# Optimization experiments

Measured on AMD Instinct MI355X. Metric: run time of the kernel, lower is better.

Reference implementation:

```python
import jax, jax.numpy as jnp
import numpy as np

DIM = 512
HEADS = 8
DK = DIM // HEADS
MAX_LEN = 22118
EPS = 1e-5


def _layernorm(h, g, b):
    m = jnp.mean(h, axis=-1, keepdims=True)
    v = jnp.mean((h - m) ** 2, axis=-1, keepdims=True)
    return (h - m) / jnp.sqrt(v + EPS) * g + b


def setup_inputs() -> dict:
    key = jax.random.key(0)
    ks = jax.random.split(key, 16)
    B, S = 4, 2048
    xavier = lambda k, shp: jax.random.normal(k, shp, jnp.float32) * np.sqrt(2.0 / (shp[0] + shp[1]))
    return {
        "x": jax.random.normal(ks[0], (B, S, DIM), jnp.float32),
        "vis_data": jax.random.normal(ks[1], (B, S, DIM), jnp.float32),
        "coord1": jax.random.randint(ks[2], (B, S), 0, MAX_LEN, jnp.int32),
        "coord2": jax.random.randint(ks[3], (B, S), 0, MAX_LEN, jnp.int32),
        "emb1": jax.random.normal(ks[4], (MAX_LEN, DIM // 2), jnp.float32) * 0.02,
        "emb2": jax.random.normal(ks[5], (MAX_LEN, DIM // 2), jnp.float32) * 0.02,
        "wq": xavier(ks[6], (DIM, DIM)), "bq": jnp.zeros((DIM,), jnp.float32),
        "wk": xavier(ks[7], (DIM, DIM)), "bk": jnp.zeros((DIM,), jnp.float32),
        "wv": xavier(ks[8], (DIM, DIM)), "bv": jnp.zeros((DIM,), jnp.float32),
        "w1": xavier(ks[9], (DIM, DIM)), "b1": jnp.zeros((DIM,), jnp.float32),
        "g1": jnp.ones((DIM,), jnp.float32), "beta1": jnp.zeros((DIM,), jnp.float32),
        "w2": xavier(ks[10], (DIM, DIM)), "b2": jnp.zeros((DIM,), jnp.float32),
        "g2": jnp.ones((DIM,), jnp.float32), "beta2": jnp.zeros((DIM,), jnp.float32),
    }


def reference(x, vis_data, coord1, coord2, emb1, emb2, wq, bq, wk, bk, wv, bv,
              w1, b1, g1, beta1, w2, b2, g2, beta2):
    B, S, _ = x.shape
    # learned positional encoding: concat of two coordinate embeddings
    pos = jnp.concatenate([emb1[coord1], emb2[coord2]], axis=-1)  # [B,S,DIM]
    xp = x + pos
    # Q/K from vis_data, V from position-encoded x
    q = (vis_data @ wq + bq).reshape(B, S, HEADS, DK)
    k = (vis_data @ wk + bk).reshape(B, S, HEADS, DK)
    v = (xp @ wv + bv).reshape(B, S, HEADS, DK)
    scores = jnp.einsum("bqhd,bkhd->bhqk", q, k) / np.sqrt(DK).astype(np.float32)
    attn = jax.nn.softmax(scores, axis=-1)  # dropout is identity in eval
    out = jnp.einsum("bhqk,bkhd->bqhd", attn, v).reshape(B, S, DIM)
    # post-attention MLP stack (self.layer)
    h = jax.nn.leaky_relu(out @ w1 + b1, negative_slope=0.2)
    h = _layernorm(h, g1, beta1)
    h = jax.nn.leaky_relu(h @ w2 + b2, negative_slope=0.2)
    h = _layernorm(h, g2, beta2)
    return h
```

## Files before the change

kernel.cpp:

```cpp
#include <hip/hip_runtime.h>

#define DIM 512
#define SEQ 2048
#define MROWS 8192

typedef short short8 __attribute__((ext_vector_type(8)));
typedef float floatx4 __attribute__((ext_vector_type(4)));

__device__ __forceinline__ ushort f2bf(float f) {
  union { float f; unsigned u; } v; v.f = f;
  unsigned r = v.u + 0x7fff + ((v.u >> 16) & 1);
  return (ushort)(r >> 16);
}
__device__ __forceinline__ float bf2f(ushort u) {
  union { unsigned u; float f; } v; v.u = ((unsigned)u) << 16;
  return v.f;
}

__global__ __launch_bounds__(256) void prep_kernel(
    const float* __restrict__ x, const float* __restrict__ vis,
    const int* __restrict__ c1, const int* __restrict__ c2,
    const float* __restrict__ e1, const float* __restrict__ e2,
    ushort* __restrict__ xp_bf, ushort* __restrict__ vis_bf) {
  int gid = blockIdx.x * 256 + threadIdx.x;
  int row = gid >> 7;
  int col = (gid & 127) * 4;
  float4 vv = *(const float4*)(vis + (size_t)row * 512 + col);
  ushort4 vb; vb.x = f2bf(vv.x); vb.y = f2bf(vv.y); vb.z = f2bf(vv.z); vb.w = f2bf(vv.w);
  *(ushort4*)(vis_bf + (size_t)row * 512 + col) = vb;
  float4 p;
  if (col < 256) p = *(const float4*)(e1 + (size_t)c1[row] * 256 + col);
  else           p = *(const float4*)(e2 + (size_t)c2[row] * 256 + col - 256);
  float4 xv = *(const float4*)(x + (size_t)row * 512 + col);
  ushort4 xb; xb.x = f2bf(xv.x + p.x); xb.y = f2bf(xv.y + p.y);
  xb.z = f2bf(xv.z + p.z); xb.w = f2bf(xv.w + p.w);
  *(ushort4*)(xp_bf + (size_t)row * 512 + col) = xb;
}

__global__ __launch_bounds__(256) void wtrans_kernel(
    const float* __restrict__ wq, const float* __restrict__ wk,
    const float* __restrict__ wv, const float* __restrict__ w1,
    const float* __restrict__ w2,
    ushort* __restrict__ wt_qkv, ushort* __restrict__ wt1,
    ushort* __restrict__ wt2) {
  __shared__ float Ls[64 * 65];
  int mid = blockIdx.x >> 6;
  int tile = blockIdx.x & 63;
  int k0 = (tile >> 3) * 64, n0 = (tile & 7) * 64;
  const float* W = mid == 0 ? wq : mid == 1 ? wk : mid == 2 ? wv : mid == 3 ? w1 : w2;
  ushort* outp = mid < 3 ? (wt_qkv + (size_t)mid * 512 * 512) : (mid == 3 ? wt1 : wt2);
  float scale = (mid == 0) ? 0.125f : 1.0f;
  int r = threadIdx.x >> 4, c4 = (threadIdx.x & 15) * 4;
#pragma unroll
  for (int i = 0; i < 4; i++) {
    int row = i * 16 + r;
    float4 wv4 = *(const float4*)(W + (size_t)(k0 + row) * 512 + n0 + c4);
    Ls[row * 65 + c4 + 0] = wv4.x * scale;
    Ls[row * 65 + c4 + 1] = wv4.y * scale;
    Ls[row * 65 + c4 + 2] = wv4.z * scale;
    Ls[row * 65 + c4 + 3] = wv4.w * scale;
  }
  __syncthreads();
  int n = threadIdx.x >> 2, kc = (threadIdx.x & 3) * 16;
  ushort pk[16];
#pragma unroll
  for (int i = 0; i < 16; i++) pk[i] = f2bf(Ls[(kc + i) * 65 + n]);
  ushort* op = outp + (size_t)(n0 + n) * 512 + k0 + kc;
  *(uint4*)op = *(uint4*)pk;
  *(uint4*)(op + 8) = *(uint4*)(pk + 8);
}

template <bool LEAKY>
__global__ __launch_bounds__(256, 3) void gemm_mfma(
    const ushort* __restrict__ A01, const ushort* __restrict__ A2,
    const ushort* __restrict__ Wt,
    const float* __restrict__ bias0, const float* __restrict__ bias1,
    const float* __restrict__ bias2,
    ushort* __restrict__ out0, ushort* __restrict__ out1,
    ushort* __restrict__ out2, float s0scale) {
  __shared__ __align__(16) ushort As[128 * 64];
  __shared__ __align__(16) ushort Bs[128 * 64];
  int t = threadIdx.x;
  int seg = blockIdx.x >> 2;
  int nloc0 = (blockIdx.x & 3) * 128;
  int n0w = blockIdx.x * 128;
  int m0 = blockIdx.y * 128;
  const ushort* A = (seg < 2) ? A01 : A2;
  const float* bias = seg == 0 ? bias0 : seg == 1 ? bias1 : bias2;
  ushort* out = seg == 0 ? out0 : seg == 1 ? out1 : out2;
  float bscale = seg == 0 ? s0scale : 1.0f;

  int w = t >> 6, lane = t & 63;
  int wm = (w & 1) * 64, wn = (w >> 1) * 64;
  int quad = lane >> 4, lcol = lane & 15;
  int srow = t >> 3, sch = t & 7;

  floatx4 acc[4][4] = {};

  for (int k0 = 0; k0 < 512; k0 += 64) {
    __syncthreads();
#pragma unroll
    for (int i = 0; i < 4; i++) {
      int row = i * 32 + srow;
      int pofs = row * 64 + (sch ^ (row & 7)) * 8;
      *(uint4*)(&As[pofs]) =
          *(const uint4*)(A + (size_t)(m0 + row) * 512 + k0 + sch * 8);
      *(uint4*)(&Bs[pofs]) =
          *(const uint4*)(Wt + (size_t)(n0w + row) * 512 + k0 + sch * 8);
    }
    __syncthreads();
#pragma unroll
    for (int kc = 0; kc < 2; kc++) {
      int pch = ((kc * 4 + quad) ^ (lcol & 7)) * 8;
      short8 af[4], bfr[4];
#pragma unroll
      for (int i = 0; i < 4; i++) {
        af[i]  = *(const short8*)(&As[(wm + i * 16 + lcol) * 64 + pch]);
        bfr[i] = *(const short8*)(&Bs[(wn + i * 16 + lcol) * 64 + pch]);
      }
#pragma unroll
      for (int mt = 0; mt < 4; mt++)
#pragma unroll
        for (int nt = 0; nt < 4; nt++)
          acc[mt][nt] = __builtin_amdgcn_mfma_f32_16x16x32_bf16(
              af[mt], bfr[nt], acc[mt][nt], 0, 0, 0);
    }
  }

  __syncthreads();
  float* Ls = ((w & 2) ? (float*)Bs : (float*)As) + (w & 1) * 1104;
  int rr = lane >> 2, cc = (lane & 3) * 16;
#pragma unroll
  for (int mt = 0; mt < 4; mt++) {
#pragma unroll
    for (int nt = 0; nt < 4; nt++) {
      float bv = bias[nloc0 + wn + nt * 16 + lcol] * bscale;
#pragma unroll
      for (int r = 0; r < 4; r++) {
        float vv = acc[mt][nt][r] + bv;
        if (LEAKY) vv = vv >= 0.f ? vv : 0.2f * vv;
        Ls[(quad * 4 + r) * 68 + nt * 16 + lcol] = vv;
      }
    }
    asm volatile("s_waitcnt lgkmcnt(0)" ::: "memory");
    ushort pk[16];
#pragma unroll
    for (int i = 0; i < 16; i += 4) {
      float4 fv = *(const float4*)(&Ls[rr * 68 + cc + i]);
      pk[i] = f2bf(fv.x); pk[i + 1] = f2bf(fv.y);
      pk[i + 2] = f2bf(fv.z); pk[i + 3] = f2bf(fv.w);
    }
    ushort* op = out + (size_t)(m0 + wm + mt * 16 + rr) * 512 + nloc0 + wn + cc;
    *(uint4*)op = *(uint4*)pk;
    *(uint4*)(op + 8) = *(uint4*)(pk + 8);
    asm volatile("s_waitcnt lgkmcnt(0)" ::: "memory");
  }
}

__global__ __launch_bounds__(256, 4) void attn_mfma_kernel(
    const ushort* __restrict__ q, const ushort* __restrict__ k,
    const ushort* __restrict__ v, ushort* __restrict__ out) {
  __shared__ __align__(16) ushort Ks[128 * 64];
  __shared__ __align__(16) ushort Vt[64 * 128];
  __shared__ __align__(16) ushort Ps[4 * 16 * 64];
  int t = threadIdx.x;
  int blk = blockIdx.x;
  int qt = blk & 31, h = (blk >> 5) & 7, b = blk >> 8;
  int wave = t >> 6, lane = t & 63, quad = lane >> 4, lcol = lane & 15;
  int q0 = qt * 64 + wave * 16;
  const size_t base = (size_t)b * SEQ * 512 + h * 64;

  short8 qf[2];
#pragma unroll
  for (int kc = 0; kc < 2; kc++)
    qf[kc] = *(const short8*)(q + base + (size_t)(q0 + lcol) * 512 + kc * 32 + quad * 8);

  floatx4 O[4] = {};
  float lsum[4] = {0.f, 0.f, 0.f, 0.f};

  ushort* Pw = Ps + wave * (16 * 64);
  int krow = t >> 1, khalf = t & 1;
  int pl = t & 63, dg = t >> 6;

  for (int kt = 0; kt < SEQ; kt += 128) {
    __syncthreads();
#pragma unroll
    for (int j = 0; j < 4; j++) {
      int ch = khalf * 4 + j;
      *(uint4*)(&Ks[krow * 64 + (ch ^ (krow & 7)) * 8]) =
          *(const uint4*)(k + base + (size_t)(kt + krow) * 512 + ch * 8);
    }
    {
      uint4 va[2], vb[2];
      const ushort* vr0 = v + base + (size_t)(kt + 2 * pl) * 512 + dg * 16;
      const ushort* vr1 = vr0 + 512;
      va[0] = *(const uint4*)(vr0); va[1] = *(const uint4*)(vr0 + 8);
      vb[0] = *(const uint4*)(vr1); vb[1] = *(const uint4*)(vr1 + 8);
      const ushort* a0 = (const ushort*)va;
      const ushort* a1 = (const ushort*)vb;
#pragma unroll
      for (int i = 0; i < 16; i++) {
        int dim = dg * 16 + i;
        unsigned pack = (unsigned)a0[i] | ((unsigned)a1[i] << 16);
        int pch = (pl >> 2) ^ (dim & 7);
        *(unsigned*)(&Vt[dim * 128 + pch * 8 + (pl & 3) * 2]) = pack;
      }
    }
    __syncthreads();

    floatx4 S[8] = {};
#pragma unroll
    for (int kc = 0; kc < 2; kc++) {
      int pch = ((kc * 4 + quad) ^ (lcol & 7)) * 8;
#pragma unroll
      for (int jt = 0; jt < 8; jt++) {
        short8 kf = *(const short8*)(&Ks[(jt * 16 + lcol) * 64 + pch]);
        S[jt] = __builtin_amdgcn_mfma_f32_16x16x32_bf16(qf[kc], kf, S[jt], 0, 0, 0);
      }
    }

#pragma unroll
    for (int half = 0; half < 2; half++) {
#pragma unroll
      for (int jt4 = 0; jt4 < 4; jt4++) {
        int jt = half * 4 + jt4;
#pragma unroll
        for (int r = 0; r < 4; r++) {
          float p = __expf(S[jt][r]);
          lsum[r] += p;
          int prow = quad * 4 + r;
          int pcol = jt4 * 16 + lcol;
          int pch = (pcol >> 3) ^ (prow & 7);
          Pw[prow * 64 + pch * 8 + (pcol & 7)] =
              (ushort)(__float_as_uint(p) >> 16);
        }
      }
      asm volatile("s_waitcnt lgkmcnt(0)" ::: "memory");
#pragma unroll
      for (int kc = 0; kc < 2; kc++) {
        short8 pf = *(const short8*)(
            &Pw[lcol * 64 + ((kc * 4 + quad) ^ (lcol & 7)) * 8]);
#pragma unroll
        for (int nt = 0; nt < 4; nt++) {
          int dim = nt * 16 + lcol;
          int ch = half * 8 + kc * 4 + quad;
          short8 vf = *(const short8*)(&Vt[dim * 128 + (ch ^ (lcol & 7)) * 8]);
          O[nt] = __builtin_amdgcn_mfma_f32_16x16x32_bf16(pf, vf, O[nt], 0, 0, 0);
        }
      }
    }
  }

#pragma unroll
  for (int r = 0; r < 4; r++) {
#pragma unroll
    for (int m = 1; m <= 8; m <<= 1) lsum[r] += __shfl_xor(lsum[r], m, 64);
    lsum[r] = 1.f / lsum[r];
  }
#pragma unroll
  for (int nt = 0; nt < 4; nt++)
#pragma unroll
    for (int r = 0; r < 4; r++)
      out[base + (size_t)(q0 + quad * 4 + r) * 512 + nt * 16 + lcol] =
          f2bf(O[nt][r] * lsum[r]);
}

template <bool OUTF32>
__global__ __launch_bounds__(256) void ln_kernel(
    const ushort* __restrict__ h, const float* __restrict__ g,
    const float* __restrict__ beta, void* __restrict__ outv) {
  int wave = threadIdx.x >> 6, lane = threadIdx.x & 63;
  int row = blockIdx.x * 4 + wave;
  uint4 raw = *(const uint4*)(h + (size_t)row * 512 + lane * 8);
  const ushort* hu = (const ushort*)&raw;
  float vals[8];
#pragma unroll
  for (int i = 0; i < 8; i++) vals[i] = bf2f(hu[i]);
  float sum = 0.f;
#pragma unroll
  for (int i = 0; i < 8; i++) sum += vals[i];
#pragma unroll
  for (int off = 32; off >= 1; off >>= 1) sum += __shfl_xor(sum, off, 64);
  float mean = sum * (1.f / 512.f);
  float vs = 0.f;
#pragma unroll
  for (int i = 0; i < 8; i++) { float d = vals[i] - mean; vs += d * d; }
#pragma unroll
  for (int off = 32; off >= 1; off >>= 1) vs += __shfl_xor(vs, off, 64);
  float rstd = rsqrtf(vs * (1.f / 512.f) + 1e-5f);
  float4 gv0 = *(const float4*)(g + lane * 8);
  float4 gv1 = *(const float4*)(g + lane * 8 + 4);
  float4 bv0 = *(const float4*)(beta + lane * 8);
  float4 bv1 = *(const float4*)(beta + lane * 8 + 4);
  float gr[8] = {gv0.x, gv0.y, gv0.z, gv0.w, gv1.x, gv1.y, gv1.z, gv1.w};
  float br[8] = {bv0.x, bv0.y, bv0.z, bv0.w, bv1.x, bv1.y, bv1.z, bv1.w};
  float res[8];
#pragma unroll
  for (int i = 0; i < 8; i++) res[i] = (vals[i] - mean) * rstd * gr[i] + br[i];
  if (OUTF32) {
    float* op = (float*)outv + (size_t)row * 512 + lane * 8;
    float4 o0, o1;
    o0.x = res[0]; o0.y = res[1]; o0.z = res[2]; o0.w = res[3];
    o1.x = res[4]; o1.y = res[5]; o1.z = res[6]; o1.w = res[7];
    *(float4*)op = o0; *(float4*)(op + 4) = o1;
  } else {
    ushort* op = (ushort*)outv + (size_t)row * 512 + lane * 8;
    ushort4 o0, o1;
    o0.x = f2bf(res[0]); o0.y = f2bf(res[1]); o0.z = f2bf(res[2]); o0.w = f2bf(res[3]);
    o1.x = f2bf(res[4]); o1.y = f2bf(res[5]); o1.z = f2bf(res[6]); o1.w = f2bf(res[7]);
    *(ushort4*)op = o0; *(ushort4*)(op + 4) = o1;
  }
}

extern "C" void kernel_launch(void* const* d_in, const int* in_sizes, int n_in,
                              void* d_out, int out_size, void* d_ws,
                              size_t ws_size, hipStream_t stream) {
  (void)in_sizes; (void)n_in; (void)out_size; (void)ws_size;
  const float* x     = (const float*)d_in[0];
  const float* vis   = (const float*)d_in[1];
  const int*   c1    = (const int*)d_in[2];
  const int*   c2    = (const int*)d_in[3];
  const float* e1    = (const float*)d_in[4];
  const float* e2    = (const float*)d_in[5];
  const float* wq    = (const float*)d_in[6];
  const float* bq    = (const float*)d_in[7];
  const float* wk    = (const float*)d_in[8];
  const float* bk    = (const float*)d_in[9];
  const float* wv    = (const float*)d_in[10];
  const float* bv    = (const float*)d_in[11];
  const float* w1    = (const float*)d_in[12];
  const float* b1    = (const float*)d_in[13];
  const float* g1    = (const float*)d_in[14];
  const float* beta1 = (const float*)d_in[15];
  const float* w2    = (const float*)d_in[16];
  const float* b2    = (const float*)d_in[17];
  const float* g2    = (const float*)d_in[18];
  const float* beta2 = (const float*)d_in[19];
  float* out = (float*)d_out;
  ushort* ws = (ushort*)d_ws;

  const size_t BUF = (size_t)MROWS * 512;
  ushort* xp_bf  = ws;
  ushort* vis_bf = ws + BUF;
  ushort* q_bf   = ws + 2 * BUF;
  ushort* k_bf   = ws + 3 * BUF;
  ushort* v_bf   = ws + 4 * BUF;
  ushort* wt_qkv = ws + 5 * BUF;
  ushort* wt1    = wt_qkv + 1536 * 512;
  ushort* wt2    = wt1 + 512 * 512;
  ushort* attn_bf = vis_bf;
  ushort* h1_bf   = xp_bf;
  ushort* ln1_bf  = q_bf;
  ushort* h2_bf   = k_bf;

  prep_kernel<<<4096, 256, 0, stream>>>(x, vis, c1, c2, e1, e2, xp_bf, vis_bf);
  wtrans_kernel<<<320, 256, 0, stream>>>(wq, wk, wv, w1, w2, wt_qkv, wt1, wt2);
  gemm_mfma<false><<<dim3(12, 64), 256, 0, stream>>>(
      vis_bf, xp_bf, wt_qkv, bq, bk, bv, q_bf, k_bf, v_bf, 0.125f);
  attn_mfma_kernel<<<1024, 256, 0, stream>>>(q_bf, k_bf, v_bf, attn_bf);
  gemm_mfma<true><<<dim3(4, 64), 256, 0, stream>>>(
      attn_bf, attn_bf, wt1, b1, b1, b1, h1_bf, h1_bf, h1_bf, 1.0f);
  ln_kernel<false><<<2048, 256, 0, stream>>>(h1_bf, g1, beta1, ln1_bf);
  gemm_mfma<true><<<dim3(4, 64), 256, 0, stream>>>(
      ln1_bf, ln1_bf, wt2, b2, b2, b2, h2_bf, h2_bf, h2_bf, 1.0f);
  ln_kernel<true><<<2048, 256, 0, stream>>>(h2_bf, g2, beta2, out);
}
```

Before: 308.1 us.

## Double attention query tile per block, shrink GEMM M-tile, merge prep kernels

The attention kernel now processes 32 query rows per wave (128 per block), so each loaded K/V tile is reused across twice as many queries and the grid is halved. In exchange it uses more registers and LDS, and its launch bound drops to 2 blocks per SM. The GEMM M-tile shrinks from 128 to 64 rows, doubling the grid, cutting LDS use and raising occupancy to 4 blocks. The prep and weight-transpose kernels are merged into one launch to remove a kernel launch.

```diff
diff --git a/kernel.cpp b/kernel.cpp
--- a/kernel.cpp
+++ b/kernel.cpp
@@ -17,109 +17,116 @@
   return v.f;
 }
 
-__global__ __launch_bounds__(256) void prep_kernel(
+__global__ __launch_bounds__(256) void prep_wtrans_kernel(
     const float* __restrict__ x, const float* __restrict__ vis,
     const int* __restrict__ c1, const int* __restrict__ c2,
     const float* __restrict__ e1, const float* __restrict__ e2,
-    ushort* __restrict__ xp_bf, ushort* __restrict__ vis_bf) {
-  int gid = blockIdx.x * 256 + threadIdx.x;
-  int row = gid >> 7;
-  int col = (gid & 127) * 4;
-  float4 vv = *(const float4*)(vis + (size_t)row * 512 + col);
-  ushort4 vb; vb.x = f2bf(vv.x); vb.y = f2bf(vv.y); vb.z = f2bf(vv.z); vb.w = f2bf(vv.w);
-  *(ushort4*)(vis_bf + (size_t)row * 512 + col) = vb;
-  float4 p;
-  if (col < 256) p = *(const float4*)(e1 + (size_t)c1[row] * 256 + col);
-  else           p = *(const float4*)(e2 + (size_t)c2[row] * 256 + col - 256);
-  float4 xv = *(const float4*)(x + (size_t)row * 512 + col);
-  ushort4 xb; xb.x = f2bf(xv.x + p.x); xb.y = f2bf(xv.y + p.y);
-  xb.z = f2bf(xv.z + p.z); xb.w = f2bf(xv.w + p.w);
-  *(ushort4*)(xp_bf + (size_t)row * 512 + col) = xb;
-}
-
-__global__ __launch_bounds__(256) void wtrans_kernel(
     const float* __restrict__ wq, const float* __restrict__ wk,
     const float* __restrict__ wv, const float* __restrict__ w1,
     const float* __restrict__ w2,
+    ushort* __restrict__ xp_bf, ushort* __restrict__ vis_bf,
     ushort* __restrict__ wt_qkv, ushort* __restrict__ wt1,
     ushort* __restrict__ wt2) {
   __shared__ float Ls[64 * 65];
-  int mid = blockIdx.x >> 6;
-  int tile = blockIdx.x & 63;
-  int k0 = (tile >> 3) * 64, n0 = (tile & 7) * 64;
-  const float* W = mid == 0 ? wq : mid == 1 ? wk : mid == 2 ? wv : mid == 3 ? w1 : w2;
-  ushort* outp = mid < 3 ? (wt_qkv + (size_t)mid * 512 * 512) : (mid == 3 ? wt1 : wt2);
-  float scale = (mid == 0) ? 0.125f : 1.0f;
-  int r = threadIdx.x >> 4, c4 = (threadIdx.x & 15) * 4;
-#pragma unroll
-  for (int i = 0; i < 4; i++) {
-    int row = i * 16 + r;
-    float4 wv4 = *(const float4*)(W + (size_t)(k0 + row) * 512 + n0 + c4);
-    Ls[row * 65 + c4 + 0] = wv4.x * scale;
-    Ls[row * 65 + c4 + 1] = wv4.y * scale;
-    Ls[row * 65 + c4 + 2] = wv4.z * scale;
-    Ls[row * 65 + c4 + 3] = wv4.w * scale;
-  }
-  __syncthreads();
-  int n = threadIdx.x >> 2, kc = (threadIdx.x & 3) * 16;
-  ushort pk[16];
-#pragma unroll
-  for (int i = 0; i < 16; i++) pk[i] = f2bf(Ls[(kc + i) * 65 + n]);
-  ushort* op = outp + (size_t)(n0 + n) * 512 + k0 + kc;
-  *(uint4*)op = *(uint4*)pk;
-  *(uint4*)(op + 8) = *(uint4*)(pk + 8);
+  if (blockIdx.x < 4096) {
+    int gid = blockIdx.x * 256 + threadIdx.x;
+    int row = gid >> 7;
+    int col = (gid & 127) * 4;
+    float4 vv = *(const float4*)(vis + (size_t)row * 512 + col);
+    ushort4 vb; vb.x = f2bf(vv.x); vb.y = f2bf(vv.y); vb.z = f2bf(vv.z); vb.w = f2bf(vv.w);
+    *(ushort4*)(vis_bf + (size_t)row * 512 + col) = vb;
+    float4 p;
+    if (col < 256) p = *(const float4*)(e1 + (size_t)c1[row] * 256 + col);
+    else           p = *(const float4*)(e2 + (size_t)c2[row] * 256 + col - 256);
+    float4 xv = *(const float4*)(x + (size_t)row * 512 + col);
+    ushort4 xb; xb.x = f2bf(xv.x + p.x); xb.y = f2bf(xv.y + p.y);
+    xb.z = f2bf(xv.z + p.z); xb.w = f2bf(xv.w + p.w);
+    *(ushort4*)(xp_bf + (size_t)row * 512 + col) = xb;
+  } else {
+    int bid = blockIdx.x - 4096;
+    int mid = bid >> 6;
+    int tile = bid & 63;
+    int k0 = (tile >> 3) * 64, n0 = (tile & 7) * 64;
+    const float* W = mid == 0 ? wq : mid == 1 ? wk : mid == 2 ? wv : mid == 3 ? w1 : w2;
+    ushort* outp = mid < 3 ? (wt_qkv + (size_t)mid * 512 * 512) : (mid == 3 ? wt1 : wt2);
+    float scale = (mid == 0) ? 0.125f : 1.0f;
+    int r = threadIdx.x >> 4, c4 = (threadIdx.x & 15) * 4;
+#pragma unroll
+    for (int i = 0; i < 4; i++) {
+      int row = i * 16 + r;
+      float4 wv4 = *(const float4*)(W + (size_t)(k0 + row) * 512 + n0 + c4);
+      Ls[row * 65 + c4 + 0] = wv4.x * scale;
+      Ls[row * 65 + c4 + 1] = wv4.y * scale;
+      Ls[row * 65 + c4 + 2] = wv4.z * scale;
+      Ls[row * 65 + c4 + 3] = wv4.w * scale;
+    }
+    __syncthreads();
+    int n = threadIdx.x >> 2, kc = (threadIdx.x & 3) * 16;
+    ushort pk[16];
+#pragma unroll
+    for (int i = 0; i < 16; i++) pk[i] = f2bf(Ls[(kc + i) * 65 + n]);
+    ushort* op = outp + (size_t)(n0 + n) * 512 + k0 + kc;
+    *(uint4*)op = *(uint4*)pk;
+    *(uint4*)(op + 8) = *(uint4*)(pk + 8);
+  }
 }
 
 template <bool LEAKY>
-__global__ __launch_bounds__(256, 3) void gemm_mfma(
+__global__ __launch_bounds__(256, 4) void gemm_mfma(
     const ushort* __restrict__ A01, const ushort* __restrict__ A2,
     const ushort* __restrict__ Wt,
     const float* __restrict__ bias0, const float* __restrict__ bias1,
     const float* __restrict__ bias2,
     ushort* __restrict__ out0, ushort* __restrict__ out1,
     ushort* __restrict__ out2, float s0scale) {
-  __shared__ __align__(16) ushort As[128 * 64];
-  __shared__ __align__(16) ushort Bs[128 * 64];
+  __shared__ __align__(16) ushort Sm[12288];
+  ushort* As = Sm;
+  ushort* Bs = Sm + 4096;
   int t = threadIdx.x;
   int seg = blockIdx.x >> 2;
   int nloc0 = (blockIdx.x & 3) * 128;
   int n0w = blockIdx.x * 128;
-  int m0 = blockIdx.y * 128;
+  int m0 = blockIdx.y * 64;
   const ushort* A = (seg < 2) ? A01 : A2;
   const float* bias = seg == 0 ? bias0 : seg == 1 ? bias1 : bias2;
   ushort* out = seg == 0 ? out0 : seg == 1 ? out1 : out2;
   float bscale = seg == 0 ? s0scale : 1.0f;
 
   int w = t >> 6, lane = t & 63;
-  int wm = (w & 1) * 64, wn = (w >> 1) * 64;
+  int wm = (w & 1) * 32, wn = (w >> 1) * 64;
   int quad = lane >> 4, lcol = lane & 15;
-  int srow = t >> 3, sch = t & 7;
-
-  floatx4 acc[4][4] = {};
+  int arow = t >> 2, ach = (t & 3) * 2;
+  int brow = t >> 1, bch = (t & 1) * 4;
+
+  floatx4 acc[2][4] = {};
 
   for (int k0 = 0; k0 < 512; k0 += 64) {
     __syncthreads();
 #pragma unroll
-    for (int i = 0; i < 4; i++) {
-      int row = i * 32 + srow;
-      int pofs = row * 64 + (sch ^ (row & 7)) * 8;
-      *(uint4*)(&As[pofs]) =
-          *(const uint4*)(A + (size_t)(m0 + row) * 512 + k0 + sch * 8);
-      *(uint4*)(&Bs[pofs]) =
-          *(const uint4*)(Wt + (size_t)(n0w + row) * 512 + k0 + sch * 8);
+    for (int i = 0; i < 2; i++) {
+      int ch = ach + i;
+      *(uint4*)(&As[arow * 64 + (ch ^ (arow & 7)) * 8]) =
+          *(const uint4*)(A + (size_t)(m0 + arow) * 512 + k0 + ch * 8);
+    }
+#pragma unroll
+    for (int j = 0; j < 4; j++) {
+      int ch = bch + j;
+      *(uint4*)(&Bs[brow * 64 + (ch ^ (brow & 7)) * 8]) =
+          *(const uint4*)(Wt + (size_t)(n0w + brow) * 512 + k0 + ch * 8);
     }
     __syncthreads();
 #pragma unroll
     for (int kc = 0; kc < 2; kc++) {
       int pch = ((kc * 4 + quad) ^ (lcol & 7)) * 8;
-      short8 af[4], bfr[4];
-#pragma unroll
-      for (int i = 0; i < 4; i++) {
-        af[i]  = *(const short8*)(&As[(wm + i * 16 + lcol) * 64 + pch]);
+      short8 af[2], bfr[4];
+#pragma unroll
+      for (int i = 0; i < 2; i++)
+        af[i] = *(const short8*)(&As[(wm + i * 16 + lcol) * 64 + pch]);
+#pragma unroll
+      for (int i = 0; i < 4; i++)
         bfr[i] = *(const short8*)(&Bs[(wn + i * 16 + lcol) * 64 + pch]);
-      }
-#pragma unroll
-      for (int mt = 0; mt < 4; mt++)
+#pragma unroll
+      for (int mt = 0; mt < 2; mt++)
 #pragma unroll
         for (int nt = 0; nt < 4; nt++)
           acc[mt][nt] = __builtin_amdgcn_mfma_f32_16x16x32_bf16(
@@ -128,10 +135,10 @@
   }
 
   __syncthreads();
-  float* Ls = ((w & 2) ? (float*)Bs : (float*)As) + (w & 1) * 1104;
+  float* Ls = (float*)Sm + w * 1088;
   int rr = lane >> 2, cc = (lane & 3) * 16;
 #pragma unroll
-  for (int mt = 0; mt < 4; mt++) {
+  for (int mt = 0; mt < 2; mt++) {
 #pragma unroll
     for (int nt = 0; nt < 4; nt++) {
       float bv = bias[nloc0 + wn + nt * 16 + lcol] * bscale;
@@ -157,28 +164,31 @@
   }
 }
 
-__global__ __launch_bounds__(256, 4) void attn_mfma_kernel(
+__global__ __launch_bounds__(256, 2) void attn_mfma_kernel(
     const ushort* __restrict__ q, const ushort* __restrict__ k,
     const ushort* __restrict__ v, ushort* __restrict__ out) {
   __shared__ __align__(16) ushort Ks[128 * 64];
   __shared__ __align__(16) ushort Vt[64 * 128];
-  __shared__ __align__(16) ushort Ps[4 * 16 * 64];
+  __shared__ __align__(16) ushort Ps[4 * 32 * 64];
   int t = threadIdx.x;
   int blk = blockIdx.x;
-  int qt = blk & 31, h = (blk >> 5) & 7, b = blk >> 8;
+  int qt = blk & 15, h = (blk >> 4) & 7, b = blk >> 7;
   int wave = t >> 6, lane = t & 63, quad = lane >> 4, lcol = lane & 15;
-  int q0 = qt * 64 + wave * 16;
+  int q0 = qt * 128 + wave * 32;
   const size_t base = (size_t)b * SEQ * 512 + h * 64;
 
-  short8 qf[2];
-#pragma unroll
-  for (int kc = 0; kc < 2; kc++)
-    qf[kc] = *(const short8*)(q + base + (size_t)(q0 + lcol) * 512 + kc * 32 + quad * 8);
-
-  floatx4 O[4] = {};
-  float lsum[4] = {0.f, 0.f, 0.f, 0.f};
-
-  ushort* Pw = Ps + wave * (16 * 64);
+  short8 qf[2][2];
+#pragma unroll
+  for (int qm = 0; qm < 2; qm++)
+#pragma unroll
+    for (int kc = 0; kc < 2; kc++)
+      qf[qm][kc] = *(const short8*)(
+          q + base + (size_t)(q0 + qm * 16 + lcol) * 512 + kc * 32 + quad * 8);
+
+  floatx4 O[2][4] = {};
+  float lsum[2][4] = {};
+
+  ushort* Pw = Ps + wave * (32 * 64);
   int krow = t >> 1, khalf = t & 1;
   int pl = t & 63, dg = t >> 6;
 
@@ -208,61 +218,72 @@
     }
     __syncthreads();
 
-    floatx4 S[8] = {};
-#pragma unroll
-    for (int kc = 0; kc < 2; kc++) {
-      int pch = ((kc * 4 + quad) ^ (lcol & 7)) * 8;
-#pragma unroll
-      for (int jt = 0; jt < 8; jt++) {
-        short8 kf = *(const short8*)(&Ks[(jt * 16 + lcol) * 64 + pch]);
-        S[jt] = __builtin_amdgcn_mfma_f32_16x16x32_bf16(qf[kc], kf, S[jt], 0, 0, 0);
+#pragma unroll
+    for (int half = 0; half < 2; half++) {
+#pragma unroll
+      for (int qm = 0; qm < 2; qm++) {
+        floatx4 S[4] = {};
+#pragma unroll
+        for (int kc = 0; kc < 2; kc++) {
+          int pch = ((kc * 4 + quad) ^ (lcol & 7)) * 8;
+#pragma unroll
+          for (int jt4 = 0; jt4 < 4; jt4++) {
+            int jrow = (half * 4 + jt4) * 16 + lcol;
+            short8 kf = *(const short8*)(&Ks[jrow * 64 + pch]);
+            S[jt4] = __builtin_amdgcn_mfma_f32_16x16x32_bf16(
+                qf[qm][kc], kf, S[jt4], 0, 0, 0);
+          }
+        }
+#pragma unroll
+        for (int jt4 = 0; jt4 < 4; jt4++)
+#pragma unroll
+          for (int r = 0; r < 4; r++) {
+            float p = __expf(S[jt4][r]);
+            lsum[qm][r] += p;
+            int prow = qm * 16 + quad * 4 + r;
+            int pcol = jt4 * 16 + lcol;
+            int pch2 = (pcol >> 3) ^ (prow & 7);
+            Pw[prow * 64 + pch2 * 8 + (pcol & 7)] =
+                (ushort)(__float_as_uint(p) >> 16);
+          }
       }
-    }
-
-#pragma unroll
-    for (int half = 0; half < 2; half++) {
-#pragma unroll
-      for (int jt4 = 0; jt4 < 4; jt4++) {
-        int jt = half * 4 + jt4;
-#pragma unroll
-        for (int r = 0; r < 4; r++) {
-          float p = __expf(S[jt][r]);
-          lsum[r] += p;
-          int prow = quad * 4 + r;
-          int pcol = jt4 * 16 + lcol;
-          int pch = (pcol >> 3) ^ (prow & 7);
-          Pw[prow * 64 + pch * 8 + (pcol & 7)] =
-              (ushort)(__float_as_uint(p) >> 16);
+      asm volatile("s_waitcnt lgkmcnt(0)" ::: "memory");
+#pragma unroll
+      for (int qm = 0; qm < 2; qm++) {
+#pragma unroll
+        for (int kc = 0; kc < 2; kc++) {
+          short8 pf = *(const short8*)(
+              &Pw[(qm * 16 + lcol) * 64 + ((kc * 4 + quad) ^ (lcol & 7)) * 8]);
+#pragma unroll
+          for (int nt = 0; nt < 4; nt++) {
+            int dim = nt * 16 + lcol;
+            int ch = half * 8 + kc * 4 + quad;
+            short8 vf = *(const short8*)(&Vt[dim * 128 + (ch ^ (lcol & 7)) * 8]);
+            O[qm][nt] = __builtin_amdgcn_mfma_f32_16x16x32_bf16(
+                pf, vf, O[qm][nt], 0, 0, 0);
+          }
         }
       }
-      asm volatile("s_waitcnt lgkmcnt(0)" ::: "memory");
-#pragma unroll
-      for (int kc = 0; kc < 2; kc++) {
-        short8 pf = *(const short8*)(
-            &Pw[lcol * 64 + ((kc * 4 + quad) ^ (lcol & 7)) * 8]);
-#pragma unroll
-        for (int nt = 0; nt < 4; nt++) {
-          int dim = nt * 16 + lcol;
-          int ch = half * 8 + kc * 4 + quad;
-          short8 vf = *(const short8*)(&Vt[dim * 128 + (ch ^ (lcol & 7)) * 8]);
-          O[nt] = __builtin_amdgcn_mfma_f32_16x16x32_bf16(pf, vf, O[nt], 0, 0, 0);
-        }
-      }
-    }
-  }
-
-#pragma unroll
-  for (int r = 0; r < 4; r++) {
-#pragma unroll
-    for (int m = 1; m <= 8; m <<= 1) lsum[r] += __shfl_xor(lsum[r], m, 64);
-    lsum[r] = 1.f / lsum[r];
-  }
-#pragma unroll
-  for (int nt = 0; nt < 4; nt++)
-#pragma unroll
-    for (int r = 0; r < 4; r++)
-      out[base + (size_t)(q0 + quad * 4 + r) * 512 + nt * 16 + lcol] =
-          f2bf(O[nt][r] * lsum[r]);
+    }
+  }
+
+#pragma unroll
+  for (int qm = 0; qm < 2; qm++)
+#pragma unroll
+    for (int r = 0; r < 4; r++) {
+#pragma unroll
+      for (int m = 1; m <= 8; m <<= 1)
+        lsum[qm][r] += __shfl_xor(lsum[qm][r], m, 64);
+      lsum[qm][r] = 1.f / lsum[qm][r];
+    }
+#pragma unroll
+  for (int qm = 0; qm < 2; qm++)
+#pragma unroll
+    for (int nt = 0; nt < 4; nt++)
+#pragma unroll
+      for (int r = 0; r < 4; r++)
+        out[base + (size_t)(q0 + qm * 16 + quad * 4 + r) * 512 + nt * 16 + lcol] =
+            f2bf(O[qm][nt][r] * lsum[qm][r]);
 }
 
 template <bool OUTF32>
@@ -353,15 +374,15 @@
   ushort* ln1_bf  = q_bf;
   ushort* h2_bf   = k_bf;
 
-  prep_kernel<<<4096, 256, 0, stream>>>(x, vis, c1, c2, e1, e2, xp_bf, vis_bf);
-  wtrans_kernel<<<320, 256, 0, stream>>>(wq, wk, wv, w1, w2, wt_qkv, wt1, wt2);
-  gemm_mfma<false><<<dim3(12, 64), 256, 0, stream>>>(
+  prep_wtrans_kernel<<<4416, 256, 0, stream>>>(
+      x, vis, c1, c2, e1, e2, wq, wk, wv, w1, w2, xp_bf, vis_bf, wt_qkv, wt1, wt2);
+  gemm_mfma<false><<<dim3(12, 128), 256, 0, stream>>>(
       vis_bf, xp_bf, wt_qkv, bq, bk, bv, q_bf, k_bf, v_bf, 0.125f);
-  attn_mfma_kernel<<<1024, 256, 0, stream>>>(q_bf, k_bf, v_bf, attn_bf);
-  gemm_mfma<true><<<dim3(4, 64), 256, 0, stream>>>(
+  attn_mfma_kernel<<<512, 256, 0, stream>>>(q_bf, k_bf, v_bf, attn_bf);
+  gemm_mfma<true><<<dim3(4, 128), 256, 0, stream>>>(
       attn_bf, attn_bf, wt1, b1, b1, b1, h1_bf, h1_bf, h1_bf, 1.0f);
   ln_kernel<false><<<2048, 256, 0, stream>>>(h1_bf, g1, beta1, ln1_bf);
-  gemm_mfma<true><<<dim3(4, 64), 256, 0, stream>>>(
+  gemm_mfma<true><<<dim3(4, 128), 256, 0, stream>>>(
       ln1_bf, ln1_bf, wt2, b2, b2, b2, h2_bf, h2_bf, h2_bf, 1.0f);
   ln_kernel<true><<<2048, 256, 0, stream>>>(h2_bf, g2, beta2, out);
 }
```

New measurement: 272.0 us. -11.7%, faster.
